# Kernel tuning notes

Hardware: AMD Instinct MI355X
Metric: run time of the kernel (lower is better)

The kernel has to match this reference:

```python
import jax, jax.numpy as jnp
import numpy as np
from jax import lax


def setup_inputs() -> dict:
    key = jax.random.key(0)
    k1, k2 = jax.random.split(key)
    L, B, D = 1024, 16, 1024
    x = jax.random.normal(k1, (L, B, D), dtype=jnp.float32)
    # weight maps n_in -> n_out*k with k=3 (n_in == n_out); small scale for stability
    weight = jax.random.normal(k2, (D, 3 * D), dtype=jnp.float32) * 0.05
    bias = jnp.zeros((2 * D,), dtype=jnp.float32)
    c0 = jnp.zeros((B, D), dtype=jnp.float32)
    return {"x": x, "weight": weight, "bias": bias, "c0": c0}


def reference(x, weight, bias, c0):
    # SRUCell forward, k == 3 (n_in == n_out), unidirectional, tanh activation,
    # no dropout masks (mask_h == NULL -> mask = 1).
    L, B, D = x.shape
    u = (x.reshape(L * B, D) @ weight).reshape(L, B, D, 3)
    b1 = bias[:D]
    b2 = bias[D:]
    u0 = u[..., 0]                                   # [L, B, D]
    g1 = jax.nn.sigmoid(u[..., 1] + b1)              # forget gate
    g2 = jax.nn.sigmoid(u[..., 2] + b2)              # reset/highway gate

    def step(c, inp):
        u0_t, g1_t, g2_t, x_t = inp
        c_new = (c - u0_t) * g1_t + u0_t             # c = c'*g1 + u0*(1-g1)
        h_t = (jnp.tanh(c_new) - x_t) * g2_t + x_t   # h = act(c)*g2 + x*(1-g2)
        return c_new, h_t

    c_last, h = lax.scan(step, c0, (u0, g1, g2, x))
    return h, c_last
```

## Files before the change

kernel.cpp:

```cpp
#include <hip/hip_runtime.h>

#define L_DIM 1024
#define B_DIM 16
#define D_DIM 1024
#define K_DIM 1024
#define N_DIM 3072
#define M_DIM (L_DIM * B_DIM)
#define CHAINS 16384
#define CHUNK 32
#define NCHUNK 32

typedef float f32x4 __attribute__((ext_vector_type(4)));
typedef __bf16 bf16x8 __attribute__((ext_vector_type(8)));
typedef unsigned short u16;
typedef unsigned int u32;

__device__ __forceinline__ u16 f2bf(float f) {
  u32 u = __float_as_uint(f);
  u = u + 0x7FFFu + ((u >> 16) & 1u);
  return (u16)(u >> 16);
}
__device__ __forceinline__ float bf2f(u16 v) {
  return __uint_as_float(((u32)v) << 16);
}
__device__ __forceinline__ float bf2f_lo(u32 v) {
  return __uint_as_float(v << 16);
}
__device__ __forceinline__ float bf2f_hi(u32 v) {
  return __uint_as_float(v & 0xffff0000u);
}
__device__ __forceinline__ float fexp(float v) {
  return __builtin_amdgcn_exp2f(v * 1.4426950408889634f);
}
__device__ __forceinline__ float sigm(float z) {
  return __builtin_amdgcn_rcpf(1.0f + fexp(-z));
}
__device__ __forceinline__ float ftanh(float v) {
  return 1.0f - 2.0f * __builtin_amdgcn_rcpf(1.0f + fexp(2.0f * v));
}

__global__ __launch_bounds__(256) void cvt_fused(const float4* __restrict__ xin,
                                                 ushort4* __restrict__ xout,
                                                 const float* __restrict__ W,
                                                 u16* __restrict__ Wt) {
  if (blockIdx.x < 16384) {
    int i = blockIdx.x * 256 + threadIdx.x;
    float4 v = xin[i];
    ushort4 o;
    o.x = f2bf(v.x); o.y = f2bf(v.y); o.z = f2bf(v.z); o.w = f2bf(v.w);
    xout[i] = o;
  } else {
    __shared__ float tile[64][65];
    int wb = blockIdx.x - 16384;
    int c0 = (wb % 48) * 64;
    int r0 = (wb / 48) * 64;
    int tx = threadIdx.x & 63;
    int ty = threadIdx.x >> 6;
#pragma unroll
    for (int i = 0; i < 16; ++i) {
      int row = i * 4 + ty;
      tile[row][tx] = W[(size_t)(r0 + row) * N_DIM + c0 + tx];
    }
    __syncthreads();
#pragma unroll
    for (int i = 0; i < 16; ++i) {
      int crow = i * 4 + ty;
      int c = c0 + crow;
      int nprime = (c % 3) * D_DIM + (c / 3);
      Wt[(size_t)nprime * K_DIM + r0 + tx] = f2bf(tile[tx][crow]);
    }
  }
}


#define AS1 __attribute__((address_space(1)))
#define AS3 __attribute__((address_space(3)))
#define STAGE(gp, lp) do { \
  __builtin_amdgcn_global_load_lds((const AS1 void*)(gp), (AS3 void*)(lp), 16, 0, 0); \
  __builtin_amdgcn_global_load_lds((const AS1 void*)((gp) + (size_t)64 * K_DIM), \
                                   (AS3 void*)((lp) + 4096), 16, 0, 0); \
} while (0)

#define QUAD(AI, JB, BF) \
  _Pragma("unroll") \
  for (int i = 0; i < 4; ++i) { \
    _Pragma("unroll") \
    for (int j = 0; j < 2; ++j) { \
      acc[AI + i][JB + j] = __builtin_amdgcn_mfma_f32_16x16x32_bf16(aF[i][0], BF[j][0], acc[AI + i][JB + j], 0, 0, 0); \
      acc[AI + i][JB + j] = __builtin_amdgcn_mfma_f32_16x16x32_bf16(aF[i][1], BF[j][1], acc[AI + i][JB + j], 0, 0, 0); \
    } \
  }

__global__ __launch_bounds__(512, 2) void gemm_kernel(const u16* __restrict__ A,
                                                      const u16* __restrict__ Bt,
                                                      u16* __restrict__ U) {
  __shared__ __align__(16) u16 sm[65536];
  const int tid = threadIdx.x;
  const int wave = tid >> 6;
  const int lane = tid & 63;
  const int wm = wave >> 2;
  const int wn = wave & 3;
  const int quad = lane >> 4;
  const int l16 = lane & 15;

  const int flat = blockIdx.y * 12 + blockIdx.x;
  const int swz = (flat & 7) * 96 + (flat >> 3);
  const int m0 = (swz / 12) * 256;
  const int n0 = (swz % 12) * 256;

  const int rr = tid >> 3;
  const int slot = (tid & 7) ^ (rr & 7);
  const u16* gA = A + (size_t)(m0 + rr) * K_DIM + slot * 8;
  const u16* gB = Bt + (size_t)(n0 + rr) * K_DIM + slot * 8;

  u16* ldsA = sm + wave * 512;
  u16* ldsB = sm + 32768 + wave * 512;

  const int swzu = (l16 & 7) << 3;
  const int c0 = (quad * 8) ^ swzu;
  const int c1 = (32 + quad * 8) ^ swzu;
  const u16* pA = sm + (wm * 128 + l16) * 64;
  const u16* pB = sm + 32768 + (wn * 64 + l16) * 64;

  f32x4 acc[8][4] = {};

  STAGE(gA, ldsA);
  STAGE(gA + (size_t)128 * K_DIM, ldsA + 8192);
  STAGE(gB, ldsB);
  STAGE(gB + (size_t)128 * K_DIM, ldsB + 8192);
  STAGE(gB + 64, ldsB + 16384);
  STAGE(gB + (size_t)128 * K_DIM + 64, ldsB + 16384 + 8192);
  asm volatile("s_waitcnt vmcnt(4)" ::: "memory");
  __builtin_amdgcn_s_barrier();

  for (int u = 0; u < 16; ++u) {
    const int buf = u & 1;
    const int nb = buf ^ 1;
    const u16* pAb = pA + buf * 16384;
    const u16* pBb = pB + buf * 16384;
    bf16x8 aF[4][2], bLo[2][2], bHi[2][2];

#pragma unroll
    for (int i = 0; i < 4; ++i) {
      aF[i][0] = *(const bf16x8*)(pAb + i * 1024 + c0);
      aF[i][1] = *(const bf16x8*)(pAb + i * 1024 + c1);
    }
#pragma unroll
    for (int j = 0; j < 2; ++j) {
      bLo[j][0] = *(const bf16x8*)(pBb + j * 1024 + c0);
      bLo[j][1] = *(const bf16x8*)(pBb + j * 1024 + c1);
      bHi[j][0] = *(const bf16x8*)(pBb + (2 + j) * 1024 + c0);
      bHi[j][1] = *(const bf16x8*)(pBb + (2 + j) * 1024 + c1);
    }
    if (u < 15) {
      STAGE(gA + (u + 1) * 64, ldsA + nb * 16384);
      STAGE(gA + (size_t)128 * K_DIM + (u + 1) * 64, ldsA + nb * 16384 + 8192);
    }
    __builtin_amdgcn_s_setprio(1);
    QUAD(0, 0, bLo)
    QUAD(0, 2, bHi)
    __builtin_amdgcn_s_setprio(0);
    __builtin_amdgcn_s_barrier();

#pragma unroll
    for (int i = 0; i < 4; ++i) {
      aF[i][0] = *(const bf16x8*)(pAb + (4 + i) * 1024 + c0);
      aF[i][1] = *(const bf16x8*)(pAb + (4 + i) * 1024 + c1);
    }
    if (u < 14) {
      STAGE(gB + (u + 2) * 64, ldsB + buf * 16384);
      STAGE(gB + (size_t)128 * K_DIM + (u + 2) * 64, ldsB + buf * 16384 + 8192);
    }
    __builtin_amdgcn_s_setprio(1);
    QUAD(4, 2, bHi)
    QUAD(4, 0, bLo)
    __builtin_amdgcn_s_setprio(0);

    if (u < 14) {
      asm volatile("s_waitcnt vmcnt(4)" ::: "memory");
    } else if (u == 14) {
      asm volatile("s_waitcnt vmcnt(0)" ::: "memory");
    }
    __builtin_amdgcn_s_barrier();
  }

#pragma unroll
  for (int i = 0; i < 8; ++i) {
#pragma unroll
    for (int j = 0; j < 4; ++j) {
      const int col = n0 + wn * 64 + j * 16 + l16;
      const int rb = m0 + wm * 128 + i * 16 + quad * 4;
#pragma unroll
      for (int r = 0; r < 4; ++r)
        U[(size_t)(rb + r) * N_DIM + col] = f2bf(acc[i][j][r]);
    }
  }
}


__global__ __launch_bounds__(1024) void sru_fused(const u16* __restrict__ U,
                                                  const float* __restrict__ x,
                                                  const float* __restrict__ bias,
                                                  const float* __restrict__ c0,
                                                  float* __restrict__ h,
                                                  float* __restrict__ clast) {
  __shared__ float sA[NCHUNK][64];
  __shared__ float sB[NCHUNK][64];
  __shared__ float sC[NCHUNK][64];

  const int flat = blockIdx.x;
  const int cb = (flat & 7) * 32 + (flat >> 3);
  const int b  = cb >> 4;
  const int d0 = (cb & 15) << 6;
  const int t  = threadIdx.x;
  const int pr = t & 31;
  const int j  = t >> 5;
  const int d2 = d0 + pr * 2;

  const float2 bb1 = *(const float2*)(bias + d2);

  {
    const u16* p = U + (size_t)(j * CHUNK * B_DIM + b) * N_DIM + d2;
    float A0 = 1.0f, A1 = 1.0f, B0 = 0.0f, B1 = 0.0f;
#pragma unroll 4
    for (int s = 0; s < CHUNK; ++s) {
      u32 w0 = *(const u32*)p;
      u32 w1 = *(const u32*)(p + D_DIM);
      float u0a = bf2f_lo(w0), u0b = bf2f_hi(w0);
      float g1a = sigm(bf2f_lo(w1) + bb1.x);
      float g1b = sigm(bf2f_hi(w1) + bb1.y);
      B0 = (B0 - u0a) * g1a + u0a;
      B1 = (B1 - u0b) * g1b + u0b;
      A0 *= g1a;
      A1 *= g1b;
      p += (size_t)B_DIM * N_DIM;
    }
    *(float2*)&sA[j][pr * 2] = make_float2(A0, A1);
    *(float2*)&sB[j][pr * 2] = make_float2(B0, B1);
  }
  __syncthreads();

  if (t < 64) {
    const int chain = cb * 64 + t;
    float c = c0[chain];
#pragma unroll
    for (int jj = 0; jj < NCHUNK; ++jj) {
      sC[jj][t] = c;
      c = sA[jj][t] * c + sB[jj][t];
    }
    clast[chain] = c;
  }
  __syncthreads();

  {
    const float2 bb2 = *(const float2*)(bias + D_DIM + d2);
    float2 c = *(const float2*)&sC[j][pr * 2];
    const size_t m0 = (size_t)(j * CHUNK * B_DIM + b);
    const u16* p = U + m0 * N_DIM + d2;
    const float* xp = x + m0 * D_DIM + d2;
    float* hp = h + m0 * D_DIM + d2;
#pragma unroll 4
    for (int s = 0; s < CHUNK; ++s) {
      u32 w0 = *(const u32*)p;
      u32 w1 = *(const u32*)(p + D_DIM);
      u32 w2 = *(const u32*)(p + 2 * D_DIM);
      float2 xv = *(const float2*)xp;
      float u0a = bf2f_lo(w0), u0b = bf2f_hi(w0);
      float g1a = sigm(bf2f_lo(w1) + bb1.x);
      float g1b = sigm(bf2f_hi(w1) + bb1.y);
      float g2a = sigm(bf2f_lo(w2) + bb2.x);
      float g2b = sigm(bf2f_hi(w2) + bb2.y);
      c.x = (c.x - u0a) * g1a + u0a;
      c.y = (c.y - u0b) * g1b + u0b;
      float2 hv;
      hv.x = (ftanh(c.x) - xv.x) * g2a + xv.x;
      hv.y = (ftanh(c.y) - xv.y) * g2b + xv.y;
      *(float2*)hp = hv;
      p += (size_t)B_DIM * N_DIM;
      xp += B_DIM * D_DIM;
      hp += B_DIM * D_DIM;
    }
  }
}

extern "C" void kernel_launch(void* const* d_in, const int* in_sizes, int n_in,
                              void* d_out, int out_size, void* d_ws, size_t ws_size,
                              hipStream_t stream) {
  const float* x = (const float*)d_in[0];
  const float* W = (const float*)d_in[1];
  const float* bias = (const float*)d_in[2];
  const float* c0 = (const float*)d_in[3];
  float* out = (float*)d_out;

  char* ws = (char*)d_ws;
  u16* xb = (u16*)ws;
  u16* wt = (u16*)(ws + 33554432);
  u16* U = (u16*)(ws + 33554432 + 6291456);

  cvt_fused<<<16384 + 768, 256, 0, stream>>>((const float4*)x, (ushort4*)xb, W, wt);
  gemm_kernel<<<dim3(N_DIM / 256, M_DIM / 256), 512, 0, stream>>>(xb, wt, U);
  sru_fused<<<256, 1024, 0, stream>>>(U, x, bias, c0, out, out + (size_t)M_DIM * D_DIM);
}
```

Before: 275.6 us.

## Replace two-pass chunked SRU scan with one-pass staged sequential scan

The old recurrence kernel read U twice: once for a per-chunk affine (A,B) reduction and again for the final pass, with a short serial combine between them. The new kernel reads U once. Each step, all threads load a 32-timestep tile into double-buffered shared memory, then 64 threads run the serial recurrence over that tile while the h output of the previous tile is written. This removes the second read of U's u0/g1 columns, but makes the serial chain cover the full sequence in only 64 threads with two barriers per tile, so latency may dominate.

```diff
diff --git a/kernel.cpp b/kernel.cpp
--- a/kernel.cpp
+++ b/kernel.cpp
@@ -7,8 +7,6 @@
 #define N_DIM 3072
 #define M_DIM (L_DIM * B_DIM)
 #define CHAINS 16384
-#define CHUNK 32
-#define NCHUNK 32
 
 typedef float f32x4 __attribute__((ext_vector_type(4)));
 typedef __bf16 bf16x8 __attribute__((ext_vector_type(8)));
@@ -198,89 +196,83 @@
 }
 
 
-__global__ __launch_bounds__(1024) void sru_fused(const u16* __restrict__ U,
-                                                  const float* __restrict__ x,
-                                                  const float* __restrict__ bias,
-                                                  const float* __restrict__ c0,
-                                                  float* __restrict__ h,
-                                                  float* __restrict__ clast) {
-  __shared__ float sA[NCHUNK][64];
-  __shared__ float sB[NCHUNK][64];
-  __shared__ float sC[NCHUNK][64];
+__global__ __launch_bounds__(1024) void sru_onepass(const u16* __restrict__ U,
+                                                    const float* __restrict__ x,
+                                                    const float* __restrict__ bias,
+                                                    const float* __restrict__ c0,
+                                                    float* __restrict__ h,
+                                                    float* __restrict__ clast) {
+  __shared__ float sU0[2][64][33];
+  __shared__ float sG1[2][64][33];
+  __shared__ float sG2[2][64][33];
+  __shared__ float sCC[2][64][33];
 
   const int flat = blockIdx.x;
   const int cb = (flat & 7) * 32 + (flat >> 3);
   const int b  = cb >> 4;
   const int d0 = (cb & 15) << 6;
   const int t  = threadIdx.x;
-  const int pr = t & 31;
-  const int j  = t >> 5;
-  const int d2 = d0 + pr * 2;
-
-  const float2 bb1 = *(const float2*)(bias + d2);
-
-  {
-    const u16* p = U + (size_t)(j * CHUNK * B_DIM + b) * N_DIM + d2;
-    float A0 = 1.0f, A1 = 1.0f, B0 = 0.0f, B1 = 0.0f;
-#pragma unroll 4
-    for (int s = 0; s < CHUNK; ++s) {
-      u32 w0 = *(const u32*)p;
-      u32 w1 = *(const u32*)(p + D_DIM);
-      float u0a = bf2f_lo(w0), u0b = bf2f_hi(w0);
-      float g1a = sigm(bf2f_lo(w1) + bb1.x);
-      float g1b = sigm(bf2f_hi(w1) + bb1.y);
-      B0 = (B0 - u0a) * g1a + u0a;
-      B1 = (B1 - u0b) * g1b + u0b;
-      A0 *= g1a;
-      A1 *= g1b;
-      p += (size_t)B_DIM * N_DIM;
-    }
-    *(float2*)&sA[j][pr * 2] = make_float2(A0, A1);
-    *(float2*)&sB[j][pr * 2] = make_float2(B0, B1);
-  }
-  __syncthreads();
-
-  if (t < 64) {
-    const int chain = cb * 64 + t;
-    float c = c0[chain];
-#pragma unroll
-    for (int jj = 0; jj < NCHUNK; ++jj) {
-      sC[jj][t] = c;
-      c = sA[jj][t] * c + sB[jj][t];
-    }
-    clast[chain] = c;
-  }
-  __syncthreads();
-
-  {
-    const float2 bb2 = *(const float2*)(bias + D_DIM + d2);
-    float2 c = *(const float2*)&sC[j][pr * 2];
-    const size_t m0 = (size_t)(j * CHUNK * B_DIM + b);
-    const u16* p = U + m0 * N_DIM + d2;
-    const float* xp = x + m0 * D_DIM + d2;
-    float* hp = h + m0 * D_DIM + d2;
-#pragma unroll 4
-    for (int s = 0; s < CHUNK; ++s) {
+  const int s  = t >> 5;
+  const int ch = (t & 31) * 2;
+
+  const float2 bb1 = *(const float2*)(bias + d0 + ch);
+  const float2 bb2 = *(const float2*)(bias + D_DIM + d0 + ch);
+
+  float creg = 0.0f;
+  if (t < 64) creg = c0[cb * 64 + t];
+
+  for (int k = 0; k <= 32; ++k) {
+    const int cur = k & 1;
+    const int prv = cur ^ 1;
+
+    if (k < 32) {
+      const size_t m = (size_t)((k * 32 + s) * 16 + b);
+      const u16* p = U + m * N_DIM + d0 + ch;
       u32 w0 = *(const u32*)p;
       u32 w1 = *(const u32*)(p + D_DIM);
       u32 w2 = *(const u32*)(p + 2 * D_DIM);
-      float2 xv = *(const float2*)xp;
-      float u0a = bf2f_lo(w0), u0b = bf2f_hi(w0);
-      float g1a = sigm(bf2f_lo(w1) + bb1.x);
-      float g1b = sigm(bf2f_hi(w1) + bb1.y);
-      float g2a = sigm(bf2f_lo(w2) + bb2.x);
-      float g2b = sigm(bf2f_hi(w2) + bb2.y);
-      c.x = (c.x - u0a) * g1a + u0a;
-      c.y = (c.y - u0b) * g1b + u0b;
+      sU0[cur][ch][s]     = bf2f_lo(w0);
+      sU0[cur][ch + 1][s] = bf2f_hi(w0);
+      sG1[cur][ch][s]     = sigm(bf2f_lo(w1) + bb1.x);
+      sG1[cur][ch + 1][s] = sigm(bf2f_hi(w1) + bb1.y);
+      sG2[cur][ch][s]     = sigm(bf2f_lo(w2) + bb2.x);
+      sG2[cur][ch + 1][s] = sigm(bf2f_hi(w2) + bb2.y);
+    }
+    if (k >= 1) {
+      const size_t m = (size_t)(((k - 1) * 32 + s) * 16 + b);
+      float ca = sCC[prv][ch][s];
+      float cbv = sCC[prv][ch + 1][s];
+      float ga = sG2[prv][ch][s];
+      float gb = sG2[prv][ch + 1][s];
+      float2 xv = *(const float2*)(x + m * D_DIM + d0 + ch);
       float2 hv;
-      hv.x = (ftanh(c.x) - xv.x) * g2a + xv.x;
-      hv.y = (ftanh(c.y) - xv.y) * g2b + xv.y;
-      *(float2*)hp = hv;
-      p += (size_t)B_DIM * N_DIM;
-      xp += B_DIM * D_DIM;
-      hp += B_DIM * D_DIM;
-    }
-  }
+      hv.x = (ftanh(ca) - xv.x) * ga + xv.x;
+      hv.y = (ftanh(cbv) - xv.y) * gb + xv.y;
+      *(float2*)(h + m * D_DIM + d0 + ch) = hv;
+    }
+    __syncthreads();
+
+    if (k < 32 && t < 64) {
+      float lu[16], lg[16];
+#pragma unroll
+      for (int q = 0; q < 16; ++q) { lu[q] = sU0[cur][t][q]; lg[q] = sG1[cur][t][q]; }
+#pragma unroll
+      for (int q = 0; q < 16; ++q) {
+        creg = (creg - lu[q]) * lg[q] + lu[q];
+        sCC[cur][t][q] = creg;
+      }
+#pragma unroll
+      for (int q = 0; q < 16; ++q) { lu[q] = sU0[cur][t][16 + q]; lg[q] = sG1[cur][t][16 + q]; }
+#pragma unroll
+      for (int q = 0; q < 16; ++q) {
+        creg = (creg - lu[q]) * lg[q] + lu[q];
+        sCC[cur][t][16 + q] = creg;
+      }
+    }
+    __syncthreads();
+  }
+
+  if (t < 64) clast[cb * 64 + t] = creg;
 }
 
 extern "C" void kernel_launch(void* const* d_in, const int* in_sizes, int n_in,
@@ -299,5 +291,5 @@
 
   cvt_fused<<<16384 + 768, 256, 0, stream>>>((const float4*)x, (ushort4*)xb, W, wt);
   gemm_kernel<<<dim3(N_DIM / 256, M_DIM / 256), 512, 0, stream>>>(xb, wt, U);
-  sru_fused<<<256, 1024, 0, stream>>>(U, x, bias, c0, out, out + (size_t)M_DIM * D_DIM);
-}
+  sru_onepass<<<256, 1024, 0, stream>>>(U, x, bias, c0, out, out + (size_t)M_DIM * D_DIM);
+}
```

Result: faster. 264.1 us (-4.2%).
